# Kernel optimization log

Measured on AMD Instinct MI355X. Metric: run time of the kernel, lower is better.

Reference implementation:

```python
import jax, jax.numpy as jnp
import numpy as np

ALPHA = 32.0
RANK = 16
SCALE = ALPHA / RANK


def setup_inputs() -> dict:
    key = jax.random.key(0)
    k1, k2, k3, k4, k5 = jax.random.split(key, 5)
    B, S, D_IN, D_OUT, N = 4, 2048, 4096, 4096, 8
    x = jax.random.normal(k1, (B, S, D_IN), dtype=jnp.float32)
    routing_w = jax.random.uniform(k2, (B, N), dtype=jnp.float32)
    W_base = jax.random.normal(k3, (D_OUT, D_IN), dtype=jnp.float32) * 0.02
    lora_down = jax.random.normal(k4, (N, RANK, D_IN), dtype=jnp.float32) * 0.02
    lora_up = jax.random.normal(k5, (N, D_OUT, RANK), dtype=jnp.float32) * 0.02
    return {"x": x, "routing_w": routing_w, "W_base": W_base,
            "lora_down": lora_down, "lora_up": lora_up}


def reference(x, routing_w, W_base, lora_down, lora_up):
    # base linear: [B,S,D_in] @ [D_out,D_in]^T -> [B,S,D_out]
    base_out = jnp.einsum('bsi,oi->bso', x, W_base)
    # per-expert LoRA down-proj: [B,S,D_in] x [N,R,D_in] -> [B,N,S,R]
    down = jnp.einsum('bsi,nri->bnsr', x, lora_down)
    # up-proj + scale: [B,N,S,R] x [N,D_out,R] -> [B,N,S,D_out]
    up = jnp.einsum('bnsr,nor->bnso', down, lora_up) * SCALE
    # routing-weighted sum over experts: [B,N] x [B,N,S,D_out] -> [B,S,D_out]
    adapter_out = jnp.einsum('bn,bnso->bso', routing_w, up)
    return base_out + adapter_out
```

## Files before the change

### kernel.cpp

```cpp
#include <hip/hip_runtime.h>
#include <hip/hip_bf16.h>
#include <stdint.h>

#define TOK    8192
#define DIN    4096
#define DOUT   4096
#define NEXP   8
#define RK     16
#define NRANK  128
#define KE     4224
#define SEQB   2048
#define LSCALE 2.0f
#define KSPLIT 4
#define KSLICE (DIN / KSPLIT)

typedef __attribute__((ext_vector_type(8))) short bf8_t;
typedef __attribute__((ext_vector_type(4))) float f4_t;

__device__ __forceinline__ void async_copy16(const void* g, void* l) {
  __builtin_amdgcn_global_load_lds((const __attribute__((address_space(1))) void*)g,
                                   (__attribute__((address_space(3))) void*)l,
                                   16, 0, 0);
}

__device__ __forceinline__ ushort f2bf(float f) {
  __hip_bfloat16 h = __float2bfloat16(f);
  return *reinterpret_cast<ushort*>(&h);
}

#define R0 (TOK * DIN / 8)
#define R1 (DOUT * DIN / 8)
#define R2 (DOUT * NEXP * 2)
#define R3 (NRANK * DIN / 8)
#define RTOT (R0 + R1 + R2 + R3)

__global__ __launch_bounds__(256)
void cvt_all_kernel(const float* __restrict__ x, const float* __restrict__ wb,
                    const float* __restrict__ lu, const float* __restrict__ ld,
                    ushort* __restrict__ Xe, ushort* __restrict__ Wc,
                    ushort* __restrict__ Ldb) {
  int i = blockIdx.x * 256 + threadIdx.x;
  const float* src;
  ushort* dst;
  if (i < R0) {
    int t = i >> 9;
    int c = (i & 511) * 8;
    src = x + (size_t)t * DIN + c;
    dst = Xe + (size_t)t * KE + c;
  } else if (i < R0 + R1) {
    int j = i - R0;
    int t = j >> 9;
    int c = (j & 511) * 8;
    src = wb + (size_t)t * DIN + c;
    dst = Wc + (size_t)t * KE + c;
  } else if (i < R0 + R1 + R2) {
    int j = i - (R0 + R1);
    int o = j >> 4;
    int rem = j & 15;
    int n = rem >> 1;
    int half = rem & 1;
    src = lu + ((size_t)n * DOUT + o) * RK + half * 8;
    dst = Wc + (size_t)o * KE + DIN + n * RK + half * 8;
  } else {
    int j = i - (R0 + R1 + R2);
    src = ld + (size_t)j * 8;
    dst = Ldb + (size_t)j * 8;
  }
  const float4* s = reinterpret_cast<const float4*>(src);
  float4 a = s[0], b = s[1];
  union { ushort u[8]; uint4 v; } o;
  o.u[0]=f2bf(a.x); o.u[1]=f2bf(a.y); o.u[2]=f2bf(a.z); o.u[3]=f2bf(a.w);
  o.u[4]=f2bf(b.x); o.u[5]=f2bf(b.y); o.u[6]=f2bf(b.z); o.u[7]=f2bf(b.w);
  *reinterpret_cast<uint4*>(dst) = o.v;
}

template<int KLEN, int LDB, int MODE>
__global__ __launch_bounds__(256)
void gemm128(const ushort* __restrict__ A,
             const ushort* __restrict__ Bm,
             float* __restrict__ C) {
  __shared__ __align__(16) ushort As[128 * 32];
  __shared__ __align__(16) ushort Bs[128 * 32];

  const int tid  = threadIdx.x;
  const int wave = tid >> 6;
  const int lane = tid & 63;

  int bm, bn;
  if (MODE == 0) {
    int bid = blockIdx.x;
    int xcd = bid & 7;
    int idx = bid >> 3;
    int nt  = xcd * 4 + (idx & 3);
    int mt  = idx >> 2;
    bm = mt * 128;
    bn = nt * 128;
  } else {
    bm = blockIdx.y * 128;
    bn = blockIdx.x * 128;
  }
  const int wm = wave & 1, wn = wave >> 1;

  f4_t acc[4][4];
#pragma unroll
  for (int i = 0; i < 4; i++)
#pragma unroll
    for (int j = 0; j < 4; j++) acc[i][j] = (f4_t){0.f, 0.f, 0.f, 0.f};

  const int f0 = tid * 8;
  const int r0 = f0 >> 5, c0 = f0 & 31;
  const int f1 = (256 + tid) * 8;
  const int r1 = f1 >> 5, c1 = f1 & 31;
  const int l0 = (wave << 6) * 8;
  const int l1 = (256 + (wave << 6)) * 8;

  const ushort* Ar = As + (wm * 64 + (lane & 15)) * 32 + (lane >> 4) * 8;
  const ushort* Br = Bs + (wn * 64 + (lane & 15)) * 32 + (lane >> 4) * 8;

  const int kbase = (MODE == 1) ? blockIdx.z * KSLICE : 0;
  const int kend  = kbase + KLEN;

  for (int k0 = kbase; k0 < kend; k0 += 32) {
    __syncthreads();
    async_copy16(A  + (size_t)(bm + r0) * KE  + k0 + c0, (void*)(As + l0));
    async_copy16(A  + (size_t)(bm + r1) * KE  + k0 + c1, (void*)(As + l1));
    async_copy16(Bm + (size_t)(bn + r0) * LDB + k0 + c0, (void*)(Bs + l0));
    async_copy16(Bm + (size_t)(bn + r1) * LDB + k0 + c1, (void*)(Bs + l1));
    __syncthreads();
    bf8_t av[4], bv[4];
#pragma unroll
    for (int i = 0; i < 4; i++) av[i] = *(const bf8_t*)(Ar + i * 16 * 32);
#pragma unroll
    for (int j = 0; j < 4; j++) bv[j] = *(const bf8_t*)(Br + j * 16 * 32);
#pragma unroll
    for (int i = 0; i < 4; i++)
#pragma unroll
      for (int j = 0; j < 4; j++)
        acc[i][j] = __builtin_amdgcn_mfma_f32_16x16x32_bf16(av[i], bv[j], acc[i][j], 0, 0, 0);
  }

  if (MODE == 0) {
#pragma unroll
    for (int i = 0; i < 4; i++) {
      int row = bm + wm * 64 + i * 16 + (lane >> 4) * 4;
#pragma unroll
      for (int j = 0; j < 4; j++) {
        int col = bn + wn * 64 + j * 16 + (lane & 15);
#pragma unroll
        for (int rr = 0; rr < 4; rr++)
          C[(size_t)(row + rr) * DOUT + col] = acc[i][j][rr];
      }
    }
  } else {
    float* Dz = C + (size_t)blockIdx.z * TOK * NRANK;
#pragma unroll
    for (int i = 0; i < 4; i++) {
      int row = bm + wm * 64 + i * 16 + (lane >> 4) * 4;
#pragma unroll
      for (int j = 0; j < 4; j++) {
        int col = wn * 64 + j * 16 + (lane & 15);
#pragma unroll
        for (int rr = 0; rr < 4; rr++)
          Dz[(size_t)(row + rr) * NRANK + col] = acc[i][j][rr];
      }
    }
  }
}

__global__ void scale_store_kernel(const float* __restrict__ D32,
                                   const float* __restrict__ rw,
                                   ushort* __restrict__ Xe) {
  int i = blockIdx.x * 256 + threadIdx.x;
  int t = i >> 5;
  int g = (i & 31) * 4;
  size_t base = (size_t)t * NRANK + g;
  const size_t ss = (size_t)TOK * NRANK;
  float4 a = *reinterpret_cast<const float4*>(D32 + base);
  float4 b = *reinterpret_cast<const float4*>(D32 + ss + base);
  float4 c = *reinterpret_cast<const float4*>(D32 + 2 * ss + base);
  float4 d = *reinterpret_cast<const float4*>(D32 + 3 * ss + base);
  int n = g >> 4;
  int bb = t / SEQB;
  float s = rw[bb * NEXP + n] * LSCALE;
  union { ushort u[4]; uint2 v; } o;
  o.u[0] = f2bf((a.x + b.x + c.x + d.x) * s);
  o.u[1] = f2bf((a.y + b.y + c.y + d.y) * s);
  o.u[2] = f2bf((a.z + b.z + c.z + d.z) * s);
  o.u[3] = f2bf((a.w + b.w + c.w + d.w) * s);
  *reinterpret_cast<uint2*>(Xe + (size_t)t * KE + DIN + g) = o.v;
}

#define BK32  32
#define NT132 (KE / BK32)

__global__ __launch_bounds__(512, 2)
void gemm256(const ushort* __restrict__ A, const ushort* __restrict__ Bm,
             float* __restrict__ C) {
  __shared__ __align__(16) ushort As[4][256 * 32];
  __shared__ __align__(16) ushort Bs[4][256 * 32];

  const int tid  = threadIdx.x;
  const int w    = tid >> 6;
  const int lane = tid & 63;
  const int wm   = w >> 2;
  const int wn   = w & 3;

  const int bid = blockIdx.x;
  const int xg  = bid & 7;
  const int j   = bid >> 3;
  const int bm  = (((xg & 3) << 3) + (j & 7)) << 8;
  const int bn  = (((xg >> 2) << 3) + (j >> 3)) << 8;

  f4_t acc[8][4];
#pragma unroll
  for (int i = 0; i < 8; ++i)
#pragma unroll
    for (int jj = 0; jj < 4; ++jj) acc[i][jj] = (f4_t){0.f, 0.f, 0.f, 0.f};

  const int frow = lane & 15;
  const int cbs  = (((lane >> 4) ^ (frow >> 1)) << 4);
  const int ar0  = wm * 128;
  const int br0  = wn * 64;

  const int sxr = (lane >> 3) << 4;
  const int t0  = (w << 10) + (lane << 4);
  const int l0b = t0 ^ sxr;
  const int l1b = (t0 + 8192) ^ sxr;
  const size_t goff0 = (size_t)(l0b >> 6) * KE + ((l0b & 63) >> 1);
  const size_t goff1 = (size_t)(l1b >> 6) * KE + ((l1b & 63) >> 1);
  const int ld0 = (w << 9);
  const int ld1 = (w << 9) + 4096;

  const ushort* Ap = A  + (size_t)bm * KE;
  const ushort* Bp = Bm + (size_t)bn * KE;

#define STAGE_A256(kt, buf) do {                                   \
    const ushort* cp_ = Ap + (size_t)(kt) * BK32;                  \
    async_copy16(cp_ + goff0, (void*)(As[buf] + ld0));             \
    async_copy16(cp_ + goff1, (void*)(As[buf] + ld1));             \
  } while (0)
#define STAGE_B256(kt, buf) do {                                   \
    const ushort* cp_ = Bp + (size_t)(kt) * BK32;                  \
    async_copy16(cp_ + goff0, (void*)(Bs[buf] + ld0));             \
    async_copy16(cp_ + goff1, (void*)(Bs[buf] + ld1));             \
  } while (0)

  STAGE_A256(0, 0); STAGE_B256(0, 0);
  STAGE_A256(1, 1); STAGE_B256(1, 1);
  asm volatile("s_waitcnt vmcnt(4)" ::: "memory");
  __builtin_amdgcn_s_barrier();

  for (int T = 0; T < NT132; ++T) {
    const int b  = T & 3;
    const int sb = (T + 2) & 3;
    const char* Ab = (const char*)As[b];
    const char* Bb = (const char*)Bs[b];
    bf8_t a0[4], a1[4], bv[4];

#pragma unroll
    for (int f = 0; f < 4; ++f)
      a0[f] = *(const bf8_t*)(Ab + (((ar0 + f * 16 + frow) << 6) ^ cbs));
#pragma unroll
    for (int g = 0; g < 4; ++g)
      bv[g] = *(const bf8_t*)(Bb + (((br0 + g * 16 + frow) << 6) ^ cbs));
#pragma unroll
    for (int f = 0; f < 4; ++f)
      a1[f] = *(const bf8_t*)(Ab + (((ar0 + 64 + f * 16 + frow) << 6) ^ cbs));
    if (T + 2 < NT132) STAGE_A256(T + 2, sb);
    __builtin_amdgcn_s_barrier();

    __builtin_amdgcn_s_setprio(1);
#pragma unroll
    for (int f = 0; f < 4; ++f)
#pragma unroll
      for (int g = 0; g < 4; ++g)
        acc[f][g] = __builtin_amdgcn_mfma_f32_16x16x32_bf16(a0[f], bv[g], acc[f][g], 0, 0, 0);
    __builtin_amdgcn_s_setprio(0);
    __builtin_amdgcn_s_barrier();

    if (T + 2 < NT132) STAGE_B256(T + 2, sb);
    __builtin_amdgcn_s_barrier();
    __builtin_amdgcn_s_setprio(1);
#pragma unroll
    for (int f = 0; f < 4; ++f)
#pragma unroll
      for (int g = 0; g < 4; ++g)
        acc[4 + f][g] = __builtin_amdgcn_mfma_f32_16x16x32_bf16(a1[f], bv[g], acc[4 + f][g], 0, 0, 0);
    __builtin_amdgcn_s_setprio(0);
    if (T < NT132 - 2)       asm volatile("s_waitcnt vmcnt(4)" ::: "memory");
    else if (T == NT132 - 2) asm volatile("s_waitcnt vmcnt(0)" ::: "memory");
    __builtin_amdgcn_s_barrier();
  }

#pragma unroll
  for (int i = 0; i < 8; ++i) {
    int row = bm + wm * 128 + i * 16 + (lane >> 4) * 4;
#pragma unroll
    for (int jj = 0; jj < 4; ++jj) {
      int col = bn + wn * 64 + jj * 16 + (lane & 15);
#pragma unroll
      for (int rr = 0; rr < 4; ++rr)
        C[(size_t)(row + rr) * DOUT + col] = acc[i][jj][rr];
    }
  }
#undef STAGE_A256
#undef STAGE_B256
}

extern "C" void kernel_launch(void* const* d_in, const int* in_sizes, int n_in,
                              void* d_out, int out_size, void* d_ws, size_t ws_size,
                              hipStream_t stream) {
  const float* x  = (const float*)d_in[0];
  const float* rw = (const float*)d_in[1];
  const float* wb = (const float*)d_in[2];
  const float* ld = (const float*)d_in[3];
  const float* lu = (const float*)d_in[4];
  float* out = (float*)d_out;

  ushort* Xe  = (ushort*)d_ws;
  ushort* Wc  = Xe + (size_t)TOK * KE;
  ushort* Ldb = Wc + (size_t)DOUT * KE;
  float*  D32 = (float*)(Ldb + (size_t)NRANK * DIN);

  cvt_all_kernel<<<RTOT / 256, 256, 0, stream>>>(x, wb, lu, ld, Xe, Wc, Ldb);

  gemm128<KSLICE, DIN, 1><<<dim3(1, TOK / 128, KSPLIT), 256, 0, stream>>>(Xe, Ldb, D32);
  scale_store_kernel<<<TOK * NRANK / 4 / 256, 256, 0, stream>>>(D32, rw, Xe);
  gemm256<<<dim3((TOK / 256) * (DOUT / 256)), 512, 0, stream>>>(Xe, Wc, out);
}
```

Before: 584.2 us.

## Restructure GEMM main loop to BK=64 double-buffered tiles with split B prefetch

Changes the 256x256 bf16 GEMM from a 4-stage ring of K=32 tiles to a 2-stage ring of K=64 tiles with a new XOR swizzle over 128-byte rows. Each iteration runs four MFMA phases and staggers the A prefetch for the next tile and the B prefetch two tiles ahead across those phases. The aim is fewer loop iterations and barriers per unit of K work, and larger contiguous global loads, while keeping LDS usage the same. The cost is more complex scheduling, B being written into the buffer the current iteration is still reading, and a changed vmcnt wait accounting that may be fragile.

```diff
diff --git a/kernel.cpp b/kernel.cpp
--- a/kernel.cpp
+++ b/kernel.cpp
@@ -190,14 +190,13 @@
   *reinterpret_cast<uint2*>(Xe + (size_t)t * KE + DIN + g) = o.v;
 }
 
-#define BK32  32
-#define NT132 (KE / BK32)
+#define NT64 (KE / 64)
 
 __global__ __launch_bounds__(512, 2)
 void gemm256(const ushort* __restrict__ A, const ushort* __restrict__ Bm,
              float* __restrict__ C) {
-  __shared__ __align__(16) ushort As[4][256 * 32];
-  __shared__ __align__(16) ushort Bs[4][256 * 32];
+  __shared__ __align__(16) ushort As2[2][256 * 64];
+  __shared__ __align__(16) ushort Bs2[2][256 * 64];
 
   const int tid  = threadIdx.x;
   const int w    = tid >> 6;
@@ -207,104 +206,128 @@
 
   const int bid = blockIdx.x;
   const int xg  = bid & 7;
-  const int j   = bid >> 3;
-  const int bm  = (((xg & 3) << 3) + (j & 7)) << 8;
-  const int bn  = (((xg >> 2) << 3) + (j >> 3)) << 8;
+  const int jj  = bid >> 3;
+  const int bm  = (((xg & 3) << 3) + (jj & 7)) << 8;
+  const int bn  = (((xg >> 2) << 3) + (jj >> 3)) << 8;
 
   f4_t acc[8][4];
 #pragma unroll
   for (int i = 0; i < 8; ++i)
 #pragma unroll
-    for (int jj = 0; jj < 4; ++jj) acc[i][jj] = (f4_t){0.f, 0.f, 0.f, 0.f};
+    for (int q = 0; q < 4; ++q) acc[i][q] = (f4_t){0.f, 0.f, 0.f, 0.f};
 
   const int frow = lane & 15;
-  const int cbs  = (((lane >> 4) ^ (frow >> 1)) << 4);
-  const int ar0  = wm * 128;
-  const int br0  = wn * 64;
-
-  const int sxr = (lane >> 3) << 4;
-  const int t0  = (w << 10) + (lane << 4);
-  const int l0b = t0 ^ sxr;
-  const int l1b = (t0 + 8192) ^ sxr;
-  const size_t goff0 = (size_t)(l0b >> 6) * KE + ((l0b & 63) >> 1);
-  const size_t goff1 = (size_t)(l1b >> 6) * KE + ((l1b & 63) >> 1);
-  const int ld0 = (w << 9);
-  const int ld1 = (w << 9) + 4096;
+  const int cb0  = (((lane >> 4) ^ (frow & 7)) << 4);
+  const int cb1  = cb0 ^ 64;
+
+  const int rr0   = w * 8 + (lane >> 3);
+  const int colst = ((lane & 7) ^ (lane >> 3)) * 8;
+  const int dst0  = w * 512;
 
   const ushort* Ap = A  + (size_t)bm * KE;
   const ushort* Bp = Bm + (size_t)bn * KE;
 
-#define STAGE_A256(kt, buf) do {                                   \
-    const ushort* cp_ = Ap + (size_t)(kt) * BK32;                  \
-    async_copy16(cp_ + goff0, (void*)(As[buf] + ld0));             \
-    async_copy16(cp_ + goff1, (void*)(As[buf] + ld1));             \
+#define STG(Mp, Ls, h, kt) do {                                              \
+    const ushort* s_ = (Mp) + (size_t)((h) * 128 + rr0) * KE                 \
+                            + (size_t)(kt) * 64 + colst;                     \
+    async_copy16(s_,                  (void*)((Ls) + (h) * 8192 + dst0));    \
+    async_copy16(s_ + (size_t)64 * KE,(void*)((Ls) + (h) * 8192 + dst0 + 4096)); \
   } while (0)
-#define STAGE_B256(kt, buf) do {                                   \
-    const ushort* cp_ = Bp + (size_t)(kt) * BK32;                  \
-    async_copy16(cp_ + goff0, (void*)(Bs[buf] + ld0));             \
-    async_copy16(cp_ + goff1, (void*)(Bs[buf] + ld1));             \
-  } while (0)
-
-  STAGE_A256(0, 0); STAGE_B256(0, 0);
-  STAGE_A256(1, 1); STAGE_B256(1, 1);
+
+  STG(Ap, As2[0], 0, 0); STG(Ap, As2[0], 1, 0);
+  STG(Bp, Bs2[0], 0, 0); STG(Bp, Bs2[0], 1, 0);
+  STG(Bp, Bs2[1], 0, 1); STG(Bp, Bs2[1], 1, 1);
   asm volatile("s_waitcnt vmcnt(4)" ::: "memory");
   __builtin_amdgcn_s_barrier();
 
-  for (int T = 0; T < NT132; ++T) {
-    const int b  = T & 3;
-    const int sb = (T + 2) & 3;
-    const char* Ab = (const char*)As[b];
-    const char* Bb = (const char*)Bs[b];
-    bf8_t a0[4], a1[4], bv[4];
-
-#pragma unroll
-    for (int f = 0; f < 4; ++f)
-      a0[f] = *(const bf8_t*)(Ab + (((ar0 + f * 16 + frow) << 6) ^ cbs));
-#pragma unroll
-    for (int g = 0; g < 4; ++g)
-      bv[g] = *(const bf8_t*)(Bb + (((br0 + g * 16 + frow) << 6) ^ cbs));
-#pragma unroll
-    for (int f = 0; f < 4; ++f)
-      a1[f] = *(const bf8_t*)(Ab + (((ar0 + 64 + f * 16 + frow) << 6) ^ cbs));
-    if (T + 2 < NT132) STAGE_A256(T + 2, sb);
-    __builtin_amdgcn_s_barrier();
-
-    __builtin_amdgcn_s_setprio(1);
-#pragma unroll
-    for (int f = 0; f < 4; ++f)
-#pragma unroll
-      for (int g = 0; g < 4; ++g)
-        acc[f][g] = __builtin_amdgcn_mfma_f32_16x16x32_bf16(a0[f], bv[g], acc[f][g], 0, 0, 0);
-    __builtin_amdgcn_s_setprio(0);
-    __builtin_amdgcn_s_barrier();
-
-    if (T + 2 < NT132) STAGE_B256(T + 2, sb);
-    __builtin_amdgcn_s_barrier();
-    __builtin_amdgcn_s_setprio(1);
-#pragma unroll
-    for (int f = 0; f < 4; ++f)
-#pragma unroll
-      for (int g = 0; g < 4; ++g)
-        acc[4 + f][g] = __builtin_amdgcn_mfma_f32_16x16x32_bf16(a1[f], bv[g], acc[4 + f][g], 0, 0, 0);
-    __builtin_amdgcn_s_setprio(0);
-    if (T < NT132 - 2)       asm volatile("s_waitcnt vmcnt(4)" ::: "memory");
-    else if (T == NT132 - 2) asm volatile("s_waitcnt vmcnt(0)" ::: "memory");
-    __builtin_amdgcn_s_barrier();
+  for (int t = 0; t < NT64; ++t) {
+    const int b = t & 1;
+    const char* Ab = (const char*)(As2[b]) + (wm * 128 + frow) * 128;
+    const char* Bb = (const char*)(Bs2[b]) + (wn * 64 + frow) * 128;
+    bf8_t bk0[4], bk1[4];
+
+    {
+      bf8_t av[4];
+#pragma unroll
+      for (int f = 0; f < 4; ++f) av[f]  = *(const bf8_t*)(Ab + f * 2048 + cb0);
+#pragma unroll
+      for (int g = 0; g < 4; ++g) bk0[g] = *(const bf8_t*)(Bb + g * 2048 + cb0);
+      if (t + 1 < NT64) { STG(Ap, As2[b ^ 1], 0, t + 1); STG(Ap, As2[b ^ 1], 1, t + 1); }
+      __builtin_amdgcn_s_barrier();
+      __builtin_amdgcn_s_setprio(1);
+#pragma unroll
+      for (int f = 0; f < 4; ++f)
+#pragma unroll
+        for (int g = 0; g < 4; ++g)
+          acc[f][g] = __builtin_amdgcn_mfma_f32_16x16x32_bf16(av[f], bk0[g], acc[f][g], 0, 0, 0);
+      __builtin_amdgcn_s_setprio(0);
+      __builtin_amdgcn_s_barrier();
+    }
+
+    {
+      bf8_t av[4];
+#pragma unroll
+      for (int f = 0; f < 4; ++f) av[f]  = *(const bf8_t*)(Ab + f * 2048 + cb1);
+#pragma unroll
+      for (int g = 0; g < 4; ++g) bk1[g] = *(const bf8_t*)(Bb + g * 2048 + cb1);
+      __builtin_amdgcn_s_barrier();
+      __builtin_amdgcn_s_setprio(1);
+#pragma unroll
+      for (int f = 0; f < 4; ++f)
+#pragma unroll
+        for (int g = 0; g < 4; ++g)
+          acc[f][g] = __builtin_amdgcn_mfma_f32_16x16x32_bf16(av[f], bk1[g], acc[f][g], 0, 0, 0);
+      __builtin_amdgcn_s_setprio(0);
+      __builtin_amdgcn_s_barrier();
+    }
+
+    {
+      bf8_t av[4];
+#pragma unroll
+      for (int f = 0; f < 4; ++f) av[f] = *(const bf8_t*)(Ab + 8192 + f * 2048 + cb0);
+      if (t + 2 < NT64) STG(Bp, Bs2[b], 0, t + 2);
+      __builtin_amdgcn_s_barrier();
+      __builtin_amdgcn_s_setprio(1);
+#pragma unroll
+      for (int f = 0; f < 4; ++f)
+#pragma unroll
+        for (int g = 0; g < 4; ++g)
+          acc[4 + f][g] = __builtin_amdgcn_mfma_f32_16x16x32_bf16(av[f], bk0[g], acc[4 + f][g], 0, 0, 0);
+      __builtin_amdgcn_s_setprio(0);
+      __builtin_amdgcn_s_barrier();
+    }
+
+    {
+      bf8_t av[4];
+#pragma unroll
+      for (int f = 0; f < 4; ++f) av[f] = *(const bf8_t*)(Ab + 8192 + f * 2048 + cb1);
+      if (t + 2 < NT64) STG(Bp, Bs2[b], 1, t + 2);
+      __builtin_amdgcn_s_barrier();
+      __builtin_amdgcn_s_setprio(1);
+#pragma unroll
+      for (int f = 0; f < 4; ++f)
+#pragma unroll
+        for (int g = 0; g < 4; ++g)
+          acc[4 + f][g] = __builtin_amdgcn_mfma_f32_16x16x32_bf16(av[f], bk1[g], acc[4 + f][g], 0, 0, 0);
+      __builtin_amdgcn_s_setprio(0);
+      if (t < NT64 - 2)       asm volatile("s_waitcnt vmcnt(4)" ::: "memory");
+      else if (t == NT64 - 2) asm volatile("s_waitcnt vmcnt(0)" ::: "memory");
+      __builtin_amdgcn_s_barrier();
+    }
   }
 
 #pragma unroll
   for (int i = 0; i < 8; ++i) {
-    int row = bm + wm * 128 + i * 16 + (lane >> 4) * 4;
-#pragma unroll
-    for (int jj = 0; jj < 4; ++jj) {
-      int col = bn + wn * 64 + jj * 16 + (lane & 15);
+    int row = bm + wm * 128 + (i >> 2) * 64 + (i & 3) * 16 + (lane >> 4) * 4;
+#pragma unroll
+    for (int q = 0; q < 4; ++q) {
+      int col = bn + wn * 64 + q * 16 + (lane & 15);
 #pragma unroll
       for (int rr = 0; rr < 4; ++rr)
-        C[(size_t)(row + rr) * DOUT + col] = acc[i][jj][rr];
-    }
-  }
-#undef STAGE_A256
-#undef STAGE_B256
+        C[(size_t)(row + rr) * DOUT + col] = acc[i][q][rr];
+    }
+  }
+#undef STG
 }
 
 extern "C" void kernel_launch(void* const* d_in, const int* in_sizes, int n_in,
```

Result: slower. 647.5 us (+10.8%).

## Software-pipeline LDS fragment reads across K iterations in gemm256

Applied to the files above, without the earlier changes.

Restructures the main GEMM loop so the next tile's A-first-half and B fragments are read from LDS during the current iteration, between the two MFMA halves, using double-buffered register fragments and a 2x manual unroll. The aim is to hide LDS read latency behind MFMA work rather than stalling at the start of each iteration. The vmcnt waits change to match the new ordering. Holding two sets of fragments raises register pressure, which could hurt occupancy at launch_bounds(512,2).

```diff
diff --git a/kernel.cpp b/kernel.cpp
--- a/kernel.cpp
+++ b/kernel.cpp
@@ -190,8 +190,7 @@
   *reinterpret_cast<uint2*>(Xe + (size_t)t * KE + DIN + g) = o.v;
 }
 
-#define BK32  32
-#define NT132 (KE / BK32)
+#define NT32 (KE / 32)
 
 __global__ __launch_bounds__(512, 2)
 void gemm256(const ushort* __restrict__ A, const ushort* __restrict__ Bm,
@@ -207,15 +206,15 @@
 
   const int bid = blockIdx.x;
   const int xg  = bid & 7;
-  const int j   = bid >> 3;
-  const int bm  = (((xg & 3) << 3) + (j & 7)) << 8;
-  const int bn  = (((xg >> 2) << 3) + (j >> 3)) << 8;
+  const int jj  = bid >> 3;
+  const int bm  = (((xg & 3) << 3) + (jj & 7)) << 8;
+  const int bn  = (((xg >> 2) << 3) + (jj >> 3)) << 8;
 
   f4_t acc[8][4];
 #pragma unroll
   for (int i = 0; i < 8; ++i)
 #pragma unroll
-    for (int jj = 0; jj < 4; ++jj) acc[i][jj] = (f4_t){0.f, 0.f, 0.f, 0.f};
+    for (int q = 0; q < 4; ++q) acc[i][q] = (f4_t){0.f, 0.f, 0.f, 0.f};
 
   const int frow = lane & 15;
   const int cbs  = (((lane >> 4) ^ (frow >> 1)) << 4);
@@ -235,76 +234,88 @@
   const ushort* Bp = Bm + (size_t)bn * KE;
 
 #define STAGE_A256(kt, buf) do {                                   \
-    const ushort* cp_ = Ap + (size_t)(kt) * BK32;                  \
+    const ushort* cp_ = Ap + (size_t)(kt) * 32;                    \
     async_copy16(cp_ + goff0, (void*)(As[buf] + ld0));             \
     async_copy16(cp_ + goff1, (void*)(As[buf] + ld1));             \
   } while (0)
 #define STAGE_B256(kt, buf) do {                                   \
-    const ushort* cp_ = Bp + (size_t)(kt) * BK32;                  \
+    const ushort* cp_ = Bp + (size_t)(kt) * 32;                    \
     async_copy16(cp_ + goff0, (void*)(Bs[buf] + ld0));             \
     async_copy16(cp_ + goff1, (void*)(Bs[buf] + ld1));             \
   } while (0)
+#define RD_A(s_, mh, f_) (*(const bf8_t*)((const char*)As[s_] + \
+    (((ar0 + (mh) * 64 + (f_) * 16 + frow) << 6) ^ cbs)))
+#define RD_B(s_, g_) (*(const bf8_t*)((const char*)Bs[s_] + \
+    (((br0 + (g_) * 16 + frow) << 6) ^ cbs)))
 
   STAGE_A256(0, 0); STAGE_B256(0, 0);
   STAGE_A256(1, 1); STAGE_B256(1, 1);
   asm volatile("s_waitcnt vmcnt(4)" ::: "memory");
   __builtin_amdgcn_s_barrier();
 
-  for (int T = 0; T < NT132; ++T) {
-    const int b  = T & 3;
-    const int sb = (T + 2) & 3;
-    const char* Ab = (const char*)As[b];
-    const char* Bb = (const char*)Bs[b];
-    bf8_t a0[4], a1[4], bv[4];
-
-#pragma unroll
-    for (int f = 0; f < 4; ++f)
-      a0[f] = *(const bf8_t*)(Ab + (((ar0 + f * 16 + frow) << 6) ^ cbs));
-#pragma unroll
-    for (int g = 0; g < 4; ++g)
-      bv[g] = *(const bf8_t*)(Bb + (((br0 + g * 16 + frow) << 6) ^ cbs));
-#pragma unroll
-    for (int f = 0; f < 4; ++f)
-      a1[f] = *(const bf8_t*)(Ab + (((ar0 + 64 + f * 16 + frow) << 6) ^ cbs));
-    if (T + 2 < NT132) STAGE_A256(T + 2, sb);
-    __builtin_amdgcn_s_barrier();
-
-    __builtin_amdgcn_s_setprio(1);
-#pragma unroll
-    for (int f = 0; f < 4; ++f)
-#pragma unroll
-      for (int g = 0; g < 4; ++g)
-        acc[f][g] = __builtin_amdgcn_mfma_f32_16x16x32_bf16(a0[f], bv[g], acc[f][g], 0, 0, 0);
-    __builtin_amdgcn_s_setprio(0);
-    __builtin_amdgcn_s_barrier();
-
-    if (T + 2 < NT132) STAGE_B256(T + 2, sb);
-    __builtin_amdgcn_s_barrier();
-    __builtin_amdgcn_s_setprio(1);
-#pragma unroll
-    for (int f = 0; f < 4; ++f)
-#pragma unroll
-      for (int g = 0; g < 4; ++g)
-        acc[4 + f][g] = __builtin_amdgcn_mfma_f32_16x16x32_bf16(a1[f], bv[g], acc[4 + f][g], 0, 0, 0);
-    __builtin_amdgcn_s_setprio(0);
-    if (T < NT132 - 2)       asm volatile("s_waitcnt vmcnt(4)" ::: "memory");
-    else if (T == NT132 - 2) asm volatile("s_waitcnt vmcnt(0)" ::: "memory");
-    __builtin_amdgcn_s_barrier();
+  bf8_t fA0[2][4], fA1[2][4], fB[2][4];
+#pragma unroll
+  for (int f = 0; f < 4; ++f) fA0[0][f] = RD_A(0, 0, f);
+#pragma unroll
+  for (int g = 0; g < 4; ++g) fB[0][g]  = RD_B(0, g);
+
+  for (int t2 = 0; t2 < NT32; t2 += 2) {
+#pragma unroll
+    for (int u = 0; u < 2; ++u) {
+      const int t  = t2 + u;
+      const int b  = t & 3;
+      const int sb = (t + 2) & 3;
+      const int b1 = (t + 1) & 3;
+
+#pragma unroll
+      for (int f = 0; f < 4; ++f) fA1[u][f] = RD_A(b, 1, f);
+      if (t + 2 < NT32) STAGE_A256(t + 2, sb);
+      __builtin_amdgcn_s_barrier();
+      __builtin_amdgcn_s_setprio(1);
+#pragma unroll
+      for (int f = 0; f < 4; ++f)
+#pragma unroll
+        for (int g = 0; g < 4; ++g)
+          acc[f][g] = __builtin_amdgcn_mfma_f32_16x16x32_bf16(fA0[u][f], fB[u][g], acc[f][g], 0, 0, 0);
+      __builtin_amdgcn_s_setprio(0);
+      __builtin_amdgcn_s_barrier();
+
+      if (t + 2 < NT32) asm volatile("s_waitcnt vmcnt(2)" ::: "memory");
+      else              asm volatile("s_waitcnt vmcnt(0)" ::: "memory");
+      if (t + 1 < NT32) {
+#pragma unroll
+        for (int f = 0; f < 4; ++f) fA0[u ^ 1][f] = RD_A(b1, 0, f);
+#pragma unroll
+        for (int g = 0; g < 4; ++g) fB[u ^ 1][g]  = RD_B(b1, g);
+      }
+      if (t + 2 < NT32) STAGE_B256(t + 2, sb);
+      __builtin_amdgcn_s_barrier();
+      __builtin_amdgcn_s_setprio(1);
+#pragma unroll
+      for (int f = 0; f < 4; ++f)
+#pragma unroll
+        for (int g = 0; g < 4; ++g)
+          acc[4 + f][g] = __builtin_amdgcn_mfma_f32_16x16x32_bf16(fA1[u][f], fB[u][g], acc[4 + f][g], 0, 0, 0);
+      __builtin_amdgcn_s_setprio(0);
+      __builtin_amdgcn_s_barrier();
+    }
   }
 
 #pragma unroll
   for (int i = 0; i < 8; ++i) {
     int row = bm + wm * 128 + i * 16 + (lane >> 4) * 4;
 #pragma unroll
-    for (int jj = 0; jj < 4; ++jj) {
-      int col = bn + wn * 64 + jj * 16 + (lane & 15);
+    for (int q = 0; q < 4; ++q) {
+      int col = bn + wn * 64 + q * 16 + (lane & 15);
 #pragma unroll
       for (int rr = 0; rr < 4; ++rr)
-        C[(size_t)(row + rr) * DOUT + col] = acc[i][jj][rr];
+        C[(size_t)(row + rr) * DOUT + col] = acc[i][q][rr];
     }
   }
 #undef STAGE_A256
 #undef STAGE_B256
+#undef RD_A
+#undef RD_B
 }
 
 extern "C" void kernel_launch(void* const* d_in, const int* in_sizes, int n_in,
```

Result: no change. 576.1 us (-1.4%).
